# Kernel optimization log

Measured on AMD Instinct MI355X. Metric: run time of the kernel, lower is better.

## Reference

```python
import jax, jax.numpy as jnp
import numpy as np

C = 684      # encoder out_channels
H = 256      # hidden_size
I = 256      # input_size (embedding dim)
A = 512      # attention dim
V = 415      # word_num (vocab)
CCOV = 256   # coverage conv channels
K = 11       # coverage conv kernel
HF, WF = 32, 128  # feature map H', W'
RATIO = 16
T = 64       # fixed number of decode steps


def gru_cell(x, h, Wih, Whh, bih, bhh):
    # torch.nn.GRUCell semantics
    gi = x @ Wih.T + bih
    gh = h @ Whh.T + bhh
    ir, iz, inn = jnp.split(gi, 3, axis=-1)
    hr, hz, hn = jnp.split(gh, 3, axis=-1)
    r = jax.nn.sigmoid(ir + hr)
    z = jax.nn.sigmoid(iz + hz)
    n = jnp.tanh(inn + r * hn)
    return (1.0 - z) * n + z * h


def setup_inputs() -> dict:
    key = jax.random.key(0)
    ks = list(jax.random.split(key, 40))
    s = 0.05
    def rn(shape):
        return jax.random.normal(ks.pop(), shape, dtype=jnp.float32) * s
    p = {}
    p['cnn_features'] = jax.random.normal(ks.pop(), (1, C, HF, WF), dtype=jnp.float32)
    p['images_mask'] = jnp.ones((1, 1, HF * RATIO, WF * RATIO), dtype=jnp.float32)
    p['emb_table'] = rn((V, I))
    p['W_init'] = rn((H, C)); p['b_init'] = jnp.zeros((H,), jnp.float32)
    p['Wih_in'] = rn((3 * H, I)); p['Whh_in'] = rn((3 * H, H))
    p['bih_in'] = jnp.zeros((3 * H,), jnp.float32); p['bhh_in'] = jnp.zeros((3 * H,), jnp.float32)
    p['Wih_out'] = rn((3 * H, C)); p['Whh_out'] = rn((3 * H, H))
    p['bih_out'] = jnp.zeros((3 * H,), jnp.float32); p['bhh_out'] = jnp.zeros((3 * H,), jnp.float32)
    p['Wq'] = rn((A, H)); p['bq'] = jnp.zeros((A,), jnp.float32)
    p['Wproj'] = rn((A, C)); p['bproj'] = jnp.zeros((A,), jnp.float32)
    p['conv_k'] = rn((CCOV, 1, K, K))
    p['Wcov'] = rn((A, CCOV))
    p['wa'] = rn((A,)); p['ba'] = jnp.zeros((), jnp.float32)
    p['Ws'] = rn((H // 2, H)); p['bs'] = jnp.zeros((H // 2,), jnp.float32)
    p['We'] = rn((H // 2, I)); p['be'] = jnp.zeros((H // 2,), jnp.float32)
    p['Wc'] = rn((H // 2, C)); p['bc'] = jnp.zeros((H // 2,), jnp.float32)
    p['Wv'] = rn((V, H // 2)); p['bv'] = jnp.zeros((V,), jnp.float32)
    return p


def _decode(cnn_features, images_mask, emb_table, W_init, b_init,
            Wih_in, Whh_in, bih_in, bhh_in, Wih_out, Whh_out, bih_out, bhh_out,
            Wq, bq, Wproj, bproj, conv_k, Wcov, wa, ba,
            Ws, bs, We, be, Wc, bc, Wv, bv):
    mask = images_mask[:, :, ::RATIO, ::RATIO]          # [1,1,HF,WF]
    avg = jnp.sum(cnn_features * mask, axis=(2, 3)) / jnp.sum(mask, axis=(2, 3))  # [1,C]
    h0 = jnp.tanh(avg @ W_init.T + b_init)               # init_hidden
    cnn_trans = jnp.einsum('bchw,ac->bhwa', cnn_features, Wproj) + bproj  # 1x1 proj, [1,HF,WF,A]
    mask2d = mask[:, 0] > 0                              # [1,HF,WF]
    emb0 = emb_table[jnp.ones((1,), dtype=jnp.int32)]    # embedding(torch.ones(1).long())
    alpha_sum0 = jnp.zeros((1, 1, HF, WF), dtype=cnn_features.dtype)

    def attend(hidden, alpha_sum):
        q = hidden @ Wq.T + bq                           # [1,A]
        cov = jax.lax.conv_general_dilated(alpha_sum, conv_k, (1, 1), [(K // 2, K // 2)] * 2)
        cov_t = jnp.einsum('bchw,ac->bhwa', cov, Wcov)   # [1,HF,WF,A]
        e = jnp.tanh(q[:, None, None, :] + cov_t + cnn_trans)
        energy = jnp.einsum('bhwa,a->bhw', e, wa) + ba
        energy = jnp.where(mask2d, energy, -1e9)
        alpha = jax.nn.softmax(energy.reshape(1, -1), axis=-1).reshape(energy.shape)
        alpha_sum = alpha_sum + alpha[:, None]
        ctx = jnp.einsum('bhw,bchw->bc', alpha, cnn_features)  # [1,C]
        return ctx, alpha_sum

    def step(carry, _):
        emb, h_par, a_sum = carry
        h1 = gru_cell(emb, h_par, Wih_in, Whh_in, bih_in, bhh_in)      # word_input_gru
        ctx, a_sum = attend(h1, a_sum)                                  # word_attention
        h = gru_cell(ctx, h1, Wih_out, Whh_out, bih_out, bhh_out)       # word_out_gru
        state = (h @ Ws.T + bs) + (emb @ We.T + be) + (ctx @ Wc.T + bc) # fused out state
        prob = state @ Wv.T + bv                                        # word_convert, [1,V]
        word = jnp.argmax(prob, axis=-1)                                # greedy feedback
        emb_next = emb_table[word]
        return (emb_next, h, a_sum), prob[0]

    _, probs = jax.lax.scan(step, (emb0, h0, alpha_sum0), None, length=T)
    return probs  # [T, V]


def reference(cnn_features, images_mask, emb_table, W_init, b_init,
              Wih_in, Whh_in, bih_in, bhh_in, Wih_out, Whh_out, bih_out, bhh_out,
              Wq, bq, Wproj, bproj, conv_k, Wcov, wa, ba,
              Ws, bs, We, be, Wc, bc, Wv, bv):
    return _decode(cnn_features, images_mask, emb_table, W_init, b_init,
                   Wih_in, Whh_in, bih_in, bhh_in, Wih_out, Whh_out, bih_out, bhh_out,
                   Wq, bq, Wproj, bproj, conv_k, Wcov, wa, ba,
                   Ws, bs, We, be, Wc, bc, Wv, bv)
```

## Files before the change

### kernel.cpp

```cpp
#include <hip/hip_runtime.h>
#include <math.h>

#define HF 32
#define WF 128
#define HW 4096
#define C_DIM 684
#define H_DIM 256
#define A_DIM 512
#define V_DIM 415
#define PADR 42
#define PADC 144
#define T_STEPS 64

#define NERG 128
#define CTX0 128
#define NCTXB 86
#define MONO 214
#define TAIL0 215
#define GIO0 231
#define PSC0 247
#define NGRID 251

constexpr int CT_OFF      = 0;
constexpr int KMT_OFF     = CT_OFF + HW * A_DIM;
constexpr int APAD_OFF    = KMT_OFF + 61952;
constexpr int MASK_OFF    = APAD_OFF + 6048;
constexpr int PART_OFF    = MASK_OFF + 4096;
constexpr int AVG_OFF     = PART_OFF + 16384;
constexpr int H0_OFF      = AVG_OFF + 704;
constexpr int QV_OFF      = H0_OFF + 256;
constexpr int H1V_OFF     = QV_OFF + 512;
constexpr int GHOV_OFF    = H1V_OFF + 512;
constexpr int GHNV_OFF    = GHOV_OFF + 1536;
constexpr int GIOV_OFF    = GHNV_OFF + 768;
constexpr int PSCV_OFF    = GIOV_OFF + 768;
constexpr int CTXV_OFF    = PSCV_OFF + 128;
constexpr int MSUM_OFF    = CTXV_OFF + 704;
constexpr int FLAGS_OFF   = MSUM_OFF + 16;
constexpr int AFR_OFF     = FLAGS_OFF + 4096;
constexpr int CR_OFF      = AFR_OFF + 128;
constexpr int H1F_OFF     = CR_OFF + 128;
constexpr int TQR_OFF     = H1F_OFF + 128;
constexpr int SYNC_INTS   = 4096 + 128 + 128 + 128 + 2048;
constexpr int SYNC_END    = FLAGS_OFF + SYNC_INTS;
constexpr int GI_OFF      = SYNC_END;
constexpr int SE_OFF      = GI_OFF + V_DIM * 768;
constexpr int WST_OFF     = SE_OFF + V_DIM * 128;
constexpr int WVT_OFF     = WST_OFF + 256 * 128;
constexpr int WS_END      = WVT_OFF + 128 * V_DIM;

__device__ __forceinline__ float sigmoidf_(float x) { return 1.f / (1.f + expf(-x)); }
__device__ __forceinline__ float ftanh(float x) {
  float e = __expf(2.f * x);
  return 1.f - 2.f / (e + 1.f);
}

__device__ __forceinline__ float gld(const float* p) {
  int v = __hip_atomic_load((const int*)p, __ATOMIC_RELAXED, __HIP_MEMORY_SCOPE_AGENT);
  return __int_as_float(v);
}
__device__ __forceinline__ void gst(float* p, float x) {
  __hip_atomic_store((int*)p, __float_as_int(x), __ATOMIC_RELAXED, __HIP_MEMORY_SCOPE_AGENT);
}
__device__ __forceinline__ void pollf(int* p, int ph) {
  int it = 0;
  while (__hip_atomic_load(p, __ATOMIC_RELAXED, __HIP_MEMORY_SCOPE_AGENT) < ph) {
    if (it < 4) __builtin_amdgcn_s_sleep(1);
    else if (it < 16) __builtin_amdgcn_s_sleep(4);
    else __builtin_amdgcn_s_sleep(8);
    ++it;
  }
  asm volatile("" ::: "memory");
}
__device__ __forceinline__ void rel_store(int* p, int v) {
  __hip_atomic_store(p, v, __ATOMIC_RELEASE, __HIP_MEMORY_SCOPE_AGENT);
}


__global__ void k_init(const float* __restrict__ imask, float* ws) {
  __shared__ float red[4];
  int tid = threadIdx.x;
  float s = 0.f;
  for (int i = tid; i < HW; i += 256) {
    int h = i >> 7, w = i & 127;
    float m = imask[h * 16 * 2048 + w * 16];
    ws[MASK_OFF + i] = m;
    s += m;
  }
  for (int i = tid; i < PADR * PADC; i += 256) ws[APAD_OFF + i] = 0.f;
  int* sync = (int*)(ws + FLAGS_OFF);
  for (int i = tid; i < SYNC_INTS; i += 256) sync[i] = 0;
#pragma unroll
  for (int off = 32; off; off >>= 1) s += __shfl_xor(s, off, 64);
  if ((tid & 63) == 0) red[tid >> 6] = s;
  __syncthreads();
  if (tid == 0) ws[MSUM_OFF] = red[0] + red[1] + red[2] + red[3];
}

__global__ void k_avg(const float* __restrict__ cnn, float* ws) {
  __shared__ float red[4];
  int c = blockIdx.x, tid = threadIdx.x;
  const float* row = cnn + c * HW;
  float s = 0.f;
  for (int i = tid; i < HW; i += 256) s += ws[MASK_OFF + i] * row[i];
#pragma unroll
  for (int off = 32; off; off >>= 1) s += __shfl_xor(s, off, 64);
  if ((tid & 63) == 0) red[tid >> 6] = s;
  __syncthreads();
  if (tid == 0) ws[AVG_OFF + c] = (red[0] + red[1] + red[2] + red[3]) / ws[MSUM_OFF];
}

__global__ void k_h0(const float* __restrict__ W_init, const float* __restrict__ b_init, float* ws) {
  __shared__ float a_s[C_DIM];
  int tid = threadIdx.x;
  for (int i = tid; i < C_DIM; i += 256) a_s[i] = ws[AVG_OFF + i];
  __syncthreads();
  const float* wr = W_init + tid * C_DIM;
  float s = b_init[tid];
  for (int k = 0; k < C_DIM; k++) s += a_s[k] * wr[k];
  ws[H0_OFF + tid] = tanhf(s);
}

__global__ __launch_bounds__(512) void k_km(const float* __restrict__ convk,
                                            const float* __restrict__ Wcov, float* ws) {
  __shared__ float kt[256];
  int t = blockIdx.x, a = threadIdx.x;
  if (a < 256) kt[a] = convk[a * 121 + t];
  __syncthreads();
  const float* wr = Wcov + a * 256;
  float s = 0.f;
  for (int c = 0; c < 256; c++) s += kt[c] * wr[c];
  ws[KMT_OFF + a * 121 + t] = s;
}

__global__ void k_ct(const float* __restrict__ cnn, const float* __restrict__ Wproj,
                     const float* __restrict__ bproj, float* ws) {
  __shared__ float As[8][128];
  __shared__ float Bs[8][64];
  int hw0 = blockIdx.x * 128;
  int a0 = blockIdx.y * 64;
  int tid = threadIdx.x;
  int tx = tid & 15, ty = tid >> 4;
  float acc[8][4];
#pragma unroll
  for (int i = 0; i < 8; i++)
#pragma unroll
    for (int j = 0; j < 4; j++) acc[i][j] = 0.f;
  for (int c0 = 0; c0 < C_DIM; c0 += 8) {
    {
      int kk = tid >> 5;
      int m4 = (tid & 31) * 4;
      int c = c0 + kk;
      float4 v = make_float4(0.f, 0.f, 0.f, 0.f);
      if (c < C_DIM) v = *(const float4*)(cnn + c * HW + hw0 + m4);
      *(float4*)&As[kk][m4] = v;
    }
    {
      int n = tid & 63;
      int kk0 = (tid >> 6) * 2;
      const float* wr = Wproj + (a0 + n) * C_DIM + c0;
      Bs[kk0][n]     = (c0 + kk0 < C_DIM) ? wr[kk0] : 0.f;
      Bs[kk0 + 1][n] = (c0 + kk0 + 1 < C_DIM) ? wr[kk0 + 1] : 0.f;
    }
    __syncthreads();
#pragma unroll
    for (int kk = 0; kk < 8; kk++) {
      float a8[8], b4[4];
#pragma unroll
      for (int i = 0; i < 8; i++) a8[i] = As[kk][ty * 8 + i];
#pragma unroll
      for (int j = 0; j < 4; j++) b4[j] = Bs[kk][tx * 4 + j];
#pragma unroll
      for (int i = 0; i < 8; i++)
#pragma unroll
        for (int j = 0; j < 4; j++) acc[i][j] += a8[i] * b4[j];
    }
    __syncthreads();
  }
#pragma unroll
  for (int i = 0; i < 8; i++) {
    int hw = hw0 + ty * 8 + i;
#pragma unroll
    for (int j = 0; j < 4; j++) {
      int a = a0 + tx * 4 + j;
      ws[CT_OFF + hw * A_DIM + a] = acc[i][j] + bproj[a];
    }
  }
}

__global__ void k_gi(const float* __restrict__ emb_table, const float* __restrict__ Wih_in,
                     const float* __restrict__ bih_in, float* ws) {
  __shared__ float e_s[256];
  int v = blockIdx.x, tid = threadIdx.x;
  e_s[tid] = emb_table[v * 256 + tid];
  __syncthreads();
#pragma unroll
  for (int r = 0; r < 3; r++) {
    int m = r * 256 + tid;
    const float* wr = Wih_in + m * 256;
    float s = bih_in[m];
    for (int k = 0; k < 256; k++) s += e_s[k] * wr[k];
    ws[GI_OFF + v * 768 + m] = s;
  }
}

__global__ void k_se(const float* __restrict__ emb_table, const float* __restrict__ We,
                     const float* __restrict__ be, float* ws) {
  __shared__ float e_s[256];
  int v = blockIdx.x, tid = threadIdx.x;
  e_s[tid] = emb_table[v * 256 + tid];
  e_s[tid + 128] = emb_table[v * 256 + tid + 128];
  __syncthreads();
  const float* wr = We + tid * 256;
  float s = be[tid];
  for (int k = 0; k < 256; k++) s += e_s[k] * wr[k];
  ws[SE_OFF + v * 128 + tid] = s;
}

__global__ void k_tr(const float* __restrict__ in, float* __restrict__ out, int M, int Kd) {
  int total = M * Kd;
  for (int i = blockIdx.x * blockDim.x + threadIdx.x; i < total; i += gridDim.x * blockDim.x) {
    int m = i / Kd, k = i - m * Kd;
    out[k * M + m] = in[i];
  }
}

__global__ __launch_bounds__(512) void k_pre0(const float* __restrict__ Whh_in,
                                              const float* __restrict__ bhh_in, float* ws) {
  __shared__ float h0s[256];
  __shared__ float ghn48[48];
  const int s = blockIdx.x, tid = threadIdx.x;
  const int j0 = s * 16;
  if (tid < 256) h0s[tid] = ws[H0_OFF + tid];
  __syncthreads();
  {
    int r = tid >> 3, l = tid & 7;
    if (r < 48) {
      int mg = (r >> 4) * 256 + j0 + (r & 15);
      const float* wr = Whh_in + mg * 256 + l * 32;
      float sm = 0.f;
#pragma unroll
      for (int k = 0; k < 32; k++) sm += h0s[l * 32 + k] * wr[k];
#pragma unroll
      for (int off = 4; off; off >>= 1) sm += __shfl_xor(sm, off, 8);
      if (l == 0) ghn48[r] = sm + bhh_in[mg];
    }
  }
  __syncthreads();
  if (tid < 16) {
    int j = j0 + tid;
    const float* gi = ws + GI_OFF + 1 * 768;
    float r = sigmoidf_(gi[j] + ghn48[tid]);
    float z = sigmoidf_(gi[256 + j] + ghn48[16 + tid]);
    float n = tanhf(gi[512 + j] + r * ghn48[32 + tid]);
    gst(ws + H1V_OFF + j, (1.f - z) * n + z * h0s[j]);
  }
}

__global__ __launch_bounds__(512) void k_pre1(const float* __restrict__ Wq,
                                              const float* __restrict__ Whh_out,
                                              const float* __restrict__ bhh_out, float* ws) {
  __shared__ float h1s[256];
  const int s = blockIdx.x, tid = threadIdx.x;
  if (tid < 256) h1s[tid] = gld(ws + H1V_OFF + tid);
  __syncthreads();
  {
    int ap = tid >> 4, l = tid & 15;
    int a = s * 32 + ap;
    const float* wr = Wq + a * 256 + l * 16;
    float sm = 0.f;
#pragma unroll
    for (int k = 0; k < 16; k++) sm += h1s[l * 16 + k] * wr[k];
#pragma unroll
    for (int off = 8; off; off >>= 1) sm += __shfl_xor(sm, off, 16);
    if (l == 0) gst(ws + QV_OFF + a, sm);
  }
  {
    int r = tid >> 3, l = tid & 7;
    if (r < 48) {
      int m = s * 48 + r;
      const float* wr = Whh_out + m * 256 + l * 32;
      float sm = 0.f;
#pragma unroll
      for (int k = 0; k < 32; k++) sm += h1s[l * 32 + k] * wr[k];
#pragma unroll
      for (int off = 4; off; off >>= 1) sm += __shfl_xor(sm, off, 8);
      if (l == 0) gst(ws + GHOV_OFF + m, sm + bhh_out[m]);
    }
  }
}

__global__ void k_go(float* ws) {
  int tid = threadIdx.x;
  if (tid < 128) ((int*)(ws + TQR_OFF))[tid * 16] = 1;
}


__global__ __launch_bounds__(512) void k_steps(
    const float* __restrict__ cnn, const float* __restrict__ Whh_in,
    const float* __restrict__ Whh_out, const float* __restrict__ Wq,
    const float* __restrict__ Wih_out, const float* __restrict__ Wc_,
    const float* __restrict__ bq, const float* __restrict__ wa, const float* __restrict__ ba,
    const float* __restrict__ bih_out, const float* __restrict__ bhh_out,
    const float* __restrict__ bhh_in,
    const float* __restrict__ bs_, const float* __restrict__ bc_, const float* __restrict__ bv_,
    float* ws, float* __restrict__ out) {
  __shared__ __align__(16) float S[40016];

  const int bid = blockIdx.x, tid = threadIdx.x;
  int* flags = (int*)(ws + FLAGS_OFF);
  int* afr   = (int*)(ws + AFR_OFF);
  int* cr    = (int*)(ws + CR_OFF);
  int* h1f   = (int*)(ws + H1F_OFF);
  int* tqr   = (int*)(ws + TQR_OFF);

  if (bid < NERG) {
    const int h_row = bid >> 2, aq = bid & 3, a0 = aq * 128;
    const int al = tid & 127, hslot = tid >> 7;
    float* km    = S;
    float* ct    = S + 16896;
    float* patch = S + 33280;
    float* maskv = S + 34864;
    float* redE  = S + 34992;
    for (int i = tid; i < 128 * 132; i += 512) {
      int a = i / 132, j = i - a * 132;
      int dy = j / 12, dx = j - dy * 12;
      km[i] = (dx < 11) ? ws[KMT_OFF + (a0 + a) * 121 + dy * 11 + dx] : 0.f;
    }
    for (int i = tid; i < 128 * 128; i += 512) {
      int w = i >> 7, aa = i & 127;
      ct[i] = ws[CT_OFF + (h_row * 128 + w) * 512 + a0 + aa];
    }
    if (tid < 128) maskv[tid] = ws[MASK_OFF + h_row * 128 + tid];
    const float bq_a = bq[a0 + al], wa_a = wa[a0 + al], ba0 = ba[0];
    __syncthreads();

#pragma unroll 1
    for (int t = 0; t < T_STEPS; t++) {
      if (tid == 0) pollf(&cr[(bid & 7) * 16], t);
      __syncthreads();
      for (int i = tid; i < 11 * 138; i += 512) {
        int r = i / 138, c = i - r * 138;
        patch[r * 144 + c] = gld(ws + APAD_OFF + (h_row + r) * PADC + c);
      }
      __syncthreads();
      float acc[2][16];
#pragma unroll
      for (int p = 0; p < 2; p++)
#pragma unroll
        for (int i = 0; i < 16; i++) acc[p][i] = 0.f;
      const int wbase0 = hslot * 32;
#pragma unroll 1
      for (int dy = 0; dy < 11; dy++) {
        float kv[12];
        {
          const float* kb = &km[al * 132 + dy * 12];
          *(float4*)&kv[0] = *(const float4*)&kb[0];
          *(float4*)&kv[4] = *(const float4*)&kb[4];
          *(float4*)&kv[8] = *(const float4*)&kb[8];
        }
#pragma unroll
        for (int p = 0; p < 2; p++) {
          float row[28];
          const float* pr = &patch[dy * 144 + wbase0 + p * 16];
#pragma unroll
          for (int i = 0; i < 7; i++) *(float4*)&row[i * 4] = *(const float4*)&pr[i * 4];
#pragma unroll
          for (int dx = 0; dx < 11; dx++)
#pragma unroll
            for (int wi = 0; wi < 16; wi++) acc[p][wi] += kv[dx] * row[wi + dx];
        }
      }
      if (tid < 16) pollf(&tqr[(tid * 8 + (bid & 7)) * 16], t + 1);
      __syncthreads();
      float qa = bq_a + gld(ws + QV_OFF + a0 + al);
#pragma unroll 1
      for (int p = 0; p < 2; p++) {
        const int wbase = wbase0 + p * 16;
#pragma unroll
        for (int wi = 0; wi < 16; wi++) {
          float x = acc[p][wi] + qa + ct[(wbase + wi) * 128 + al];
          float v = ftanh(x) * wa_a;
#pragma unroll
          for (int off = 32; off; off >>= 1) v += __shfl_xor(v, off, 64);
          if ((tid & 63) == 0) redE[(tid >> 6) * 16 + wi] = v;
        }
        __syncthreads();
        if (tid < 64) {
          int hs2 = tid >> 4, wi = tid & 15;
          int w = hs2 * 32 + p * 16 + wi;
          float e = redE[(hs2 * 2) * 16 + wi] + redE[(hs2 * 2 + 1) * 16 + wi];
          float val = (maskv[w] > 0.f) ? (e + (aq == 0 ? ba0 : 0.f)) : -2.5e8f;
          gst(ws + PART_OFF + aq * 4096 + h_row * 128 + w, val);
        }
        __syncthreads();
      }
      if (tid == 0) rel_store(&flags[bid * 16], t + 1);
    }

  } else if (bid < CTX0 + NCTXB) {
    const int cb = bid - CTX0, c0 = cb * 8;
    float* cnnS = S;
    float* redC = S + 32768;
    float* ctxv = S + 32832;
    float* invp = S + 32840;
    for (int i = tid; i < 8 * 4096; i += 512) {
      int c = c0 + (i >> 12);
      cnnS[i] = (c < C_DIM) ? cnn[c * 4096 + (i & 4095)] : 0.f;
    }
    __syncthreads();

#pragma unroll 1
    for (int t = 0; t < T_STEPS; t++) {
      if (tid == 0) pollf(&afr[(bid & 7) * 16], t + 1);
      __syncthreads();
      float ev[8];
      float ssum = 0.f;
#pragma unroll
      for (int j = 0; j < 8; j++) {
        int hw = j * 512 + tid;
        float e = gld(ws + PART_OFF + hw) + gld(ws + PART_OFF + 4096 + hw) +
                  gld(ws + PART_OFF + 8192 + hw) + gld(ws + PART_OFF + 12288 + hw);
        ev[j] = __expf(e);
        ssum += ev[j];
      }
#pragma unroll
      for (int off = 32; off; off >>= 1) ssum += __shfl_xor(ssum, off, 64);
      if ((tid & 63) == 0) redC[tid >> 6] = ssum;
      __syncthreads();
      if (tid == 0) {
        float s2 = 0.f;
#pragma unroll
        for (int i = 0; i < 8; i++) s2 += redC[i];
        invp[0] = 1.f / s2;
      }
      __syncthreads();
      float inv = invp[0];
      if (cb < 8) {
        int hw = cb * 512 + tid;
        int hh = hw >> 7, ww = hw & 127;
        float* ap = ws + APAD_OFF + (hh + 5) * PADC + ww + 5;
        gst(ap, gld(ap) + ev[cb] * inv);
      }
#pragma unroll
      for (int cc = 0; cc < 8; cc++) {
        float p = 0.f;
#pragma unroll
        for (int j = 0; j < 8; j++) p += ev[j] * cnnS[cc * 4096 + j * 512 + tid];
#pragma unroll
        for (int off = 32; off; off >>= 1) p += __shfl_xor(p, off, 64);
        if ((tid & 63) == 0) redC[(tid >> 6) * 8 + cc] = p;
      }
      __syncthreads();
      if (tid < 8) {
        float cv = 0.f;
#pragma unroll
        for (int w2 = 0; w2 < 8; w2++) cv += redC[w2 * 8 + tid];
        gst(ws + CTXV_OFF + c0 + tid, cv * inv);
      }
      __syncthreads();
      if (tid == 0) rel_store(&flags[(CTX0 + cb) * 16], t + 1);
    }

  } else if (bid == MONO) {
    float* wst  = S;
    float* mh   = S + 32768;
    float* mst  = S + 33024;
    float* wval = S + 33152;
    int*   widx = (int*)(S + 33160);
    int*   mwp  = (int*)(S + 33168);
    int*   mwn  = (int*)(S + 33169);
    for (int i = tid; i < 256 * 128; i += 512) wst[i] = ws[WST_OFF + i];
    if (tid == 0) mwp[0] = 1;
    __syncthreads();

#pragma unroll 1
    for (int t = 0; t < T_STEPS; t++) {
      const int par = t & 1;
      if (tid < 128) pollf(&flags[tid * 16], t + 1);
      __syncthreads();
      if (tid < 8) rel_store(&afr[tid * 16], t + 1);
      float o0 = 0.f, o1 = 0.f, o2 = 0.f, h1v = 0.f;
      if (tid < 256) {
        const float* gh = ws + GHOV_OFF + par * 768;
        o0 = gld(gh + tid);
        o1 = gld(gh + 256 + tid);
        o2 = gld(gh + 512 + tid);
        h1v = gld(ws + H1V_OFF + par * 256 + tid);
      }
      if (tid < NCTXB) pollf(&flags[(CTX0 + tid) * 16], t + 1);
      __syncthreads();
      if (tid < 8) rel_store(&cr[tid * 16], t + 1);
      if (tid < 16) pollf(&flags[(230 + tid) * 16], t + 1);
      else if (tid < 20) pollf(&flags[(246 + tid - 16) * 16], t + 1);
      __syncthreads();
      if (tid < 256) {
        float g0 = gld(ws + GIOV_OFF + tid);
        float g1 = gld(ws + GIOV_OFF + 256 + tid);
        float g2 = gld(ws + GIOV_OFF + 512 + tid);
        float r = sigmoidf_(g0 + o0);
        float z = sigmoidf_(g1 + o1);
        float n = tanhf(g2 + r * o2);
        mh[tid] = (1.f - z) * n + z * h1v;
      }
      __syncthreads();
      if (tid < 128) {
        float s = bs_[tid] + bc_[tid] + ws[SE_OFF + mwp[0] * 128 + tid] +
                  gld(ws + PSCV_OFF + tid);
        const float* wt = wst + tid;
#pragma unroll 8
        for (int k = 0; k < 256; k++) s += mh[k] * wt[k * 128];
        mst[tid] = s;
      }
      __syncthreads();
      {
        float best = -3.4e38f;
        int bi = tid;
        if (tid < V_DIM) {
          float p2 = bv_[tid];
          const float* wt = ws + WVT_OFF + tid;
#pragma unroll 8
          for (int k = 0; k < 128; k++) p2 += mst[k] * wt[k * V_DIM];
          out[t * V_DIM + tid] = p2;
          best = p2;
        }
#pragma unroll
        for (int off = 32; off; off >>= 1) {
          float ov = __shfl_xor(best, off, 64);
          int oi = __shfl_xor(bi, off, 64);
          if (ov > best || (ov == best && oi < bi)) { best = ov; bi = oi; }
        }
        if ((tid & 63) == 0) { wval[tid >> 6] = best; widx[tid >> 6] = bi; }
        __syncthreads();
        if (tid == 0) {
          float b0 = wval[0];
          int i0 = widx[0];
          for (int w2 = 1; w2 < 8; w2++) {
            if (wval[w2] > b0 || (wval[w2] == b0 && widx[w2] < i0)) {
              b0 = wval[w2];
              i0 = widx[w2];
            }
          }
          mwn[0] = i0;
        }
        __syncthreads();
      }
      if (tid < 16) pollf(&flags[(214 + tid) * 16], t + 1);
      __syncthreads();
      if (tid < 256) {
        const float* gi = ws + GI_OFF + mwn[0] * 768;
        float n0 = gld(ws + GHNV_OFF + tid);
        float n1 = gld(ws + GHNV_OFF + 256 + tid);
        float n2 = gld(ws + GHNV_OFF + 512 + tid);
        float r = sigmoidf_(gi[tid] + n0);
        float z = sigmoidf_(gi[256 + tid] + n1);
        float n = tanhf(gi[512 + tid] + r * n2);
        gst(ws + H1V_OFF + ((t + 1) & 1) * 256 + tid, (1.f - z) * n + z * mh[tid]);
      }
      __syncthreads();
      if (tid < 8) rel_store(&h1f[tid * 16], t + 1);
      if (tid == 0) mwp[0] = mwn[0];
      __syncthreads();
    }

  } else if (bid < GIO0) {
    const int s = bid - TAIL0;
    float* whinS = S;
    float* whoS  = S + 12672;
    float* wqS   = S + 25344;
    float* hS    = S + 33792;
    float* h1S   = S + 34048;
    for (int i = tid; i < 48 * 256; i += 512) whinS[(i >> 8) * 264 + (i & 255)] = Whh_in[s * 12288 + i];
    for (int i = tid; i < 48 * 256; i += 512) whoS[(i >> 8) * 264 + (i & 255)] = Whh_out[s * 12288 + i];
    for (int i = tid; i < 32 * 256; i += 512) wqS[(i >> 8) * 264 + (i & 255)] = Wq[s * 8192 + i];
    __syncthreads();

#pragma unroll 1
    for (int t = 0; t < T_STEPS; t++) {
      const int par = t & 1;
      if (tid < 16) pollf(&flags[(230 + tid) * 16], t + 1);
      __syncthreads();
      if (tid < 256) {
        float g0 = gld(ws + GIOV_OFF + tid);
        float g1 = gld(ws + GIOV_OFF + 256 + tid);
        float g2 = gld(ws + GIOV_OFF + 512 + tid);
        const float* gh = ws + GHOV_OFF + par * 768;
        float o0 = gld(gh + tid), o1 = gld(gh + 256 + tid), o2 = gld(gh + 512 + tid);
        float h1v = gld(ws + H1V_OFF + par * 256 + tid);
        float r = sigmoidf_(g0 + o0);
        float z = sigmoidf_(g1 + o1);
        float n = tanhf(g2 + r * o2);
        hS[tid] = (1.f - z) * n + z * h1v;
      }
      __syncthreads();
      {
        int r = tid >> 3, l = tid & 7;
        if (r < 48) {
          int m = s * 48 + r;
          float sm = 0.f;
#pragma unroll
          for (int jj = 0; jj < 8; jj++) {
            float4 w4 = *(const float4*)&whinS[r * 264 + jj * 32 + l * 4];
            float4 h4 = *(const float4*)&hS[jj * 32 + l * 4];
            sm += w4.x * h4.x + w4.y * h4.y + w4.z * h4.z + w4.w * h4.w;
          }
#pragma unroll
          for (int off = 4; off; off >>= 1) sm += __shfl_xor(sm, off, 8);
          if (l == 0) gst(ws + GHNV_OFF + m, sm + bhh_in[m]);
        }
      }
      __syncthreads();
      if (tid == 0) rel_store(&flags[(214 + s) * 16], t + 1);
      if (tid == 0) pollf(&h1f[(s & 7) * 16], t + 1);
      __syncthreads();
      if (tid < 256) h1S[tid] = gld(ws + H1V_OFF + ((t + 1) & 1) * 256 + tid);
      __syncthreads();
      {
        int r = tid >> 3, l = tid & 7;
        if (r < 48) {
          int m = s * 48 + r;
          float sm = 0.f;
#pragma unroll
          for (int jj = 0; jj < 8; jj++) {
            float4 w4 = *(const float4*)&whoS[r * 264 + jj * 32 + l * 4];
            float4 h4 = *(const float4*)&h1S[jj * 32 + l * 4];
            sm += w4.x * h4.x + w4.y * h4.y + w4.z * h4.z + w4.w * h4.w;
          }
#pragma unroll
          for (int off = 4; off; off >>= 1) sm += __shfl_xor(sm, off, 8);
          if (l == 0) gst(ws + GHOV_OFF + ((t + 1) & 1) * 768 + m, sm + bhh_out[m]);
        }
      }
      {
        int ap = tid >> 4, l = tid & 15;
        int a = s * 32 + ap;
        float sm = 0.f;
#pragma unroll
        for (int jj = 0; jj < 4; jj++) {
          float4 w4 = *(const float4*)&wqS[ap * 264 + jj * 64 + l * 4];
          float4 h4 = *(const float4*)&h1S[jj * 64 + l * 4];
          sm += w4.x * h4.x + w4.y * h4.y + w4.z * h4.z + w4.w * h4.w;
        }
#pragma unroll
        for (int off = 8; off; off >>= 1) sm += __shfl_xor(sm, off, 16);
        if (l == 0) gst(ws + QV_OFF + a, sm);
      }
      __syncthreads();
      if (tid < 8) rel_store(&tqr[(s * 8 + tid) * 16], t + 2);
    }

  } else if (bid < PSC0) {
    const int g = bid - GIO0;
    float* wS  = S;
    float* cvS = S + 33120;
    for (int i = tid; i < 48 * 684; i += 512) {
      int r = i / 684, c = i - r * 684;
      wS[r * 690 + c] = Wih_out[(g * 48 + r) * 684 + c];
    }
    __syncthreads();
#pragma unroll 1
    for (int t = 0; t < T_STEPS; t++) {
      if (tid == 0) pollf(&cr[(bid & 7) * 16], t + 1);
      __syncthreads();
      for (int i = tid; i < 684; i += 512) cvS[i] = gld(ws + CTXV_OFF + i);
      __syncthreads();
      {
        int r = tid >> 3, l = tid & 7;
        if (r < 48) {
          float sm = 0.f;
          for (int k = l; k < 684; k += 8) sm += wS[r * 690 + k] * cvS[k];
#pragma unroll
          for (int off = 4; off; off >>= 1) sm += __shfl_xor(sm, off, 8);
          if (l == 0) {
            int m = g * 48 + r;
            gst(ws + GIOV_OFF + m, sm + bih_out[m]);
          }
        }
      }
      __syncthreads();
      if (tid == 0) rel_store(&flags[(230 + g) * 16], t + 1);
    }

  } else {
    const int p = bid - PSC0;
    float* wS  = S;
    float* cvS = S + 22080;
    for (int i = tid; i < 32 * 684; i += 512) {
      int r = i / 684, c = i - r * 684;
      wS[r * 690 + c] = Wc_[(p * 32 + r) * 684 + c];
    }
    __syncthreads();
#pragma unroll 1
    for (int t = 0; t < T_STEPS; t++) {
      if (tid == 0) pollf(&cr[(bid & 7) * 16], t + 1);
      __syncthreads();
      for (int i = tid; i < 684; i += 512) cvS[i] = gld(ws + CTXV_OFF + i);
      __syncthreads();
      {
        int r = tid >> 4, l = tid & 15;
        if (r < 32) {
          float sm = 0.f;
          for (int k = l; k < 684; k += 16) sm += wS[r * 690 + k] * cvS[k];
#pragma unroll
          for (int off = 8; off; off >>= 1) sm += __shfl_xor(sm, off, 16);
          if (l == 0) gst(ws + PSCV_OFF + p * 32 + r, sm);
        }
      }
      __syncthreads();
      if (tid == 0) rel_store(&flags[(246 + p) * 16], t + 1);
    }
  }
}


extern "C" void kernel_launch(void* const* d_in, const int* in_sizes, int n_in,
                              void* d_out, int out_size, void* d_ws, size_t ws_size,
                              hipStream_t stream) {
  (void)in_sizes; (void)n_in; (void)out_size; (void)ws_size;
  const float* cnn      = (const float*)d_in[0];
  const float* imask    = (const float*)d_in[1];
  const float* emb_tab  = (const float*)d_in[2];
  const float* W_init   = (const float*)d_in[3];
  const float* b_init   = (const float*)d_in[4];
  const float* Wih_in   = (const float*)d_in[5];
  const float* Whh_in   = (const float*)d_in[6];
  const float* bih_in   = (const float*)d_in[7];
  const float* bhh_in   = (const float*)d_in[8];
  const float* Wih_out  = (const float*)d_in[9];
  const float* Whh_out  = (const float*)d_in[10];
  const float* bih_out  = (const float*)d_in[11];
  const float* bhh_out  = (const float*)d_in[12];
  const float* Wq       = (const float*)d_in[13];
  const float* bq       = (const float*)d_in[14];
  const float* Wproj    = (const float*)d_in[15];
  const float* bproj    = (const float*)d_in[16];
  const float* convk    = (const float*)d_in[17];
  const float* Wcov     = (const float*)d_in[18];
  const float* Ws_      = (const float*)d_in[21];
  const float* bs_      = (const float*)d_in[22];
  const float* We_      = (const float*)d_in[23];
  const float* be_      = (const float*)d_in[24];
  const float* Wc_      = (const float*)d_in[25];
  const float* bc_      = (const float*)d_in[26];
  const float* Wv_      = (const float*)d_in[27];
  const float* bv_      = (const float*)d_in[28];
  const float* wa       = (const float*)d_in[19];
  const float* ba       = (const float*)d_in[20];
  float* ws  = (float*)d_ws;
  float* out = (float*)d_out;

  k_init<<<1, 256, 0, stream>>>(imask, ws);
  k_avg<<<C_DIM, 256, 0, stream>>>(cnn, ws);
  k_h0<<<1, 256, 0, stream>>>(W_init, b_init, ws);
  k_km<<<121, 512, 0, stream>>>(convk, Wcov, ws);
  k_ct<<<dim3(HW / 128, A_DIM / 64), 256, 0, stream>>>(cnn, Wproj, bproj, ws);
  k_gi<<<V_DIM, 256, 0, stream>>>(emb_tab, Wih_in, bih_in, ws);
  k_se<<<V_DIM, 128, 0, stream>>>(emb_tab, We_, be_, ws);
  k_tr<<<512, 256, 0, stream>>>(Ws_, ws + WST_OFF, 128, 256);
  k_tr<<<512, 256, 0, stream>>>(Wv_, ws + WVT_OFF, 415, 128);
  k_pre0<<<16, 512, 0, stream>>>(Whh_in, bhh_in, ws);
  k_pre1<<<16, 512, 0, stream>>>(Wq, Whh_out, bhh_out, ws);
  k_go<<<1, 256, 0, stream>>>(ws);

  k_steps<<<NGRID, 512, 0, stream>>>(cnn, Whh_in, Whh_out, Wq, Wih_out, Wc_,
                                     bq, wa, ba, bih_out, bhh_out, bhh_in,
                                     bs_, bc_, bv_, ws, out);
}
```

Before: 2.750 ms.

## Replace relay-based step barriers with direct replicated producer flags

Removes the MONO block's relay stage, where it polled all energy and context flags and then republished them as aggregate flags. Energy blocks now write 8 replicated flags, which context blocks poll directly. Context blocks write 8 replicated flags, which the GRU-gate, psc and MONO blocks poll directly. This cuts a serial hop from each step's critical path, at the cost of more flag stores and wider polling per block.

```diff
diff --git a/kernel.cpp b/kernel.cpp
--- a/kernel.cpp
+++ b/kernel.cpp
@@ -36,13 +36,16 @@
 constexpr int PSCV_OFF    = GIOV_OFF + 768;
 constexpr int CTXV_OFF    = PSCV_OFF + 128;
 constexpr int MSUM_OFF    = CTXV_OFF + 704;
-constexpr int FLAGS_OFF   = MSUM_OFF + 16;
-constexpr int AFR_OFF     = FLAGS_OFF + 4096;
-constexpr int CR_OFF      = AFR_OFF + 128;
-constexpr int H1F_OFF     = CR_OFF + 128;
-constexpr int TQR_OFF     = H1F_OFF + 128;
-constexpr int SYNC_INTS   = 4096 + 128 + 128 + 128 + 2048;
-constexpr int SYNC_END    = FLAGS_OFF + SYNC_INTS;
+constexpr int EFR_OFF     = MSUM_OFF + 16;
+constexpr int CFR_OFF     = EFR_OFF + 1024 * 16;
+constexpr int TF_OFF      = CFR_OFF + 688 * 16;
+constexpr int GF_OFF      = TF_OFF + 16 * 16;
+constexpr int PSCF_OFF    = GF_OFF + 16 * 16;
+constexpr int CR_OFF      = PSCF_OFF + 4 * 16;
+constexpr int H1F_OFF     = CR_OFF + 8 * 16;
+constexpr int TQR_OFF     = H1F_OFF + 8 * 16;
+constexpr int SYNC_INTS   = (1024 + 688 + 16 + 16 + 4 + 8 + 8 + 128) * 16;
+constexpr int SYNC_END    = EFR_OFF + SYNC_INTS;
 constexpr int GI_OFF      = SYNC_END;
 constexpr int SE_OFF      = GI_OFF + V_DIM * 768;
 constexpr int WST_OFF     = SE_OFF + V_DIM * 128;
@@ -88,7 +91,7 @@
     s += m;
   }
   for (int i = tid; i < PADR * PADC; i += 256) ws[APAD_OFF + i] = 0.f;
-  int* sync = (int*)(ws + FLAGS_OFF);
+  int* sync = (int*)(ws + EFR_OFF);
   for (int i = tid; i < SYNC_INTS; i += 256) sync[i] = 0;
 #pragma unroll
   for (int off = 32; off; off >>= 1) s += __shfl_xor(s, off, 64);
@@ -308,11 +311,14 @@
   __shared__ __align__(16) float S[40016];
 
   const int bid = blockIdx.x, tid = threadIdx.x;
-  int* flags = (int*)(ws + FLAGS_OFF);
-  int* afr   = (int*)(ws + AFR_OFF);
-  int* cr    = (int*)(ws + CR_OFF);
-  int* h1f   = (int*)(ws + H1F_OFF);
-  int* tqr   = (int*)(ws + TQR_OFF);
+  int* efr  = (int*)(ws + EFR_OFF);
+  int* cfr  = (int*)(ws + CFR_OFF);
+  int* tf   = (int*)(ws + TF_OFF);
+  int* gf   = (int*)(ws + GF_OFF);
+  int* pscf = (int*)(ws + PSCF_OFF);
+  int* cr   = (int*)(ws + CR_OFF);
+  int* h1f  = (int*)(ws + H1F_OFF);
+  int* tqr  = (int*)(ws + TQR_OFF);
 
   if (bid < NERG) {
     const int h_row = bid >> 2, aq = bid & 3, a0 = aq * 128;
@@ -395,7 +401,7 @@
         }
         __syncthreads();
       }
-      if (tid == 0) rel_store(&flags[bid * 16], t + 1);
+      if (tid < 8) rel_store(&efr[(bid * 8 + tid) * 16], t + 1);
     }
 
   } else if (bid < CTX0 + NCTXB) {
@@ -412,7 +418,7 @@
 
 #pragma unroll 1
     for (int t = 0; t < T_STEPS; t++) {
-      if (tid == 0) pollf(&afr[(bid & 7) * 16], t + 1);
+      if (tid < 128) pollf(&efr[(tid * 8 + (cb & 7)) * 16], t + 1);
       __syncthreads();
       float ev[8];
       float ssum = 0.f;
@@ -459,7 +465,7 @@
         gst(ws + CTXV_OFF + c0 + tid, cv * inv);
       }
       __syncthreads();
-      if (tid == 0) rel_store(&flags[(CTX0 + cb) * 16], t + 1);
+      if (tid < 8) rel_store(&cfr[(cb * 8 + tid) * 16], t + 1);
     }
 
   } else if (bid == MONO) {
@@ -477,9 +483,9 @@
 #pragma unroll 1
     for (int t = 0; t < T_STEPS; t++) {
       const int par = t & 1;
-      if (tid < 128) pollf(&flags[tid * 16], t + 1);
-      __syncthreads();
-      if (tid < 8) rel_store(&afr[tid * 16], t + 1);
+      if (tid < NCTXB) pollf(&cfr[(tid * 8 + 7) * 16], t + 1);
+      __syncthreads();
+      if (tid < 8) rel_store(&cr[tid * 16], t + 1);
       float o0 = 0.f, o1 = 0.f, o2 = 0.f, h1v = 0.f;
       if (tid < 256) {
         const float* gh = ws + GHOV_OFF + par * 768;
@@ -488,11 +494,8 @@
         o2 = gld(gh + 512 + tid);
         h1v = gld(ws + H1V_OFF + par * 256 + tid);
       }
-      if (tid < NCTXB) pollf(&flags[(CTX0 + tid) * 16], t + 1);
-      __syncthreads();
-      if (tid < 8) rel_store(&cr[tid * 16], t + 1);
-      if (tid < 16) pollf(&flags[(230 + tid) * 16], t + 1);
-      else if (tid < 20) pollf(&flags[(246 + tid - 16) * 16], t + 1);
+      if (tid < 16) pollf(&gf[tid * 16], t + 1);
+      else if (tid < 20) pollf(&pscf[(tid - 16) * 16], t + 1);
       __syncthreads();
       if (tid < 256) {
         float g0 = gld(ws + GIOV_OFF + tid);
@@ -545,7 +548,7 @@
         }
         __syncthreads();
       }
-      if (tid < 16) pollf(&flags[(214 + tid) * 16], t + 1);
+      if (tid < 16) pollf(&tf[tid * 16], t + 1);
       __syncthreads();
       if (tid < 256) {
         const float* gi = ws + GI_OFF + mwn[0] * 768;
@@ -578,7 +581,7 @@
 #pragma unroll 1
     for (int t = 0; t < T_STEPS; t++) {
       const int par = t & 1;
-      if (tid < 16) pollf(&flags[(230 + tid) * 16], t + 1);
+      if (tid < 16) pollf(&gf[tid * 16], t + 1);
       __syncthreads();
       if (tid < 256) {
         float g0 = gld(ws + GIOV_OFF + tid);
@@ -610,7 +613,7 @@
         }
       }
       __syncthreads();
-      if (tid == 0) rel_store(&flags[(214 + s) * 16], t + 1);
+      if (tid == 0) rel_store(&tf[s * 16], t + 1);
       if (tid == 0) pollf(&h1f[(s & 7) * 16], t + 1);
       __syncthreads();
       if (tid < 256) h1S[tid] = gld(ws + H1V_OFF + ((t + 1) & 1) * 256 + tid);
@@ -660,7 +663,7 @@
     __syncthreads();
 #pragma unroll 1
     for (int t = 0; t < T_STEPS; t++) {
-      if (tid == 0) pollf(&cr[(bid & 7) * 16], t + 1);
+      if (tid < NCTXB) pollf(&cfr[(tid * 8 + (bid & 7)) * 16], t + 1);
       __syncthreads();
       for (int i = tid; i < 684; i += 512) cvS[i] = gld(ws + CTXV_OFF + i);
       __syncthreads();
@@ -678,7 +681,7 @@
         }
       }
       __syncthreads();
-      if (tid == 0) rel_store(&flags[(230 + g) * 16], t + 1);
+      if (tid == 0) rel_store(&gf[g * 16], t + 1);
     }
 
   } else {
@@ -692,7 +695,7 @@
     __syncthreads();
 #pragma unroll 1
     for (int t = 0; t < T_STEPS; t++) {
-      if (tid == 0) pollf(&cr[(bid & 7) * 16], t + 1);
+      if (tid < NCTXB) pollf(&cfr[(tid * 8 + (bid & 7)) * 16], t + 1);
       __syncthreads();
       for (int i = tid; i < 684; i += 512) cvS[i] = gld(ws + CTXV_OFF + i);
       __syncthreads();
@@ -707,7 +710,7 @@
         }
       }
       __syncthreads();
-      if (tid == 0) rel_store(&flags[(246 + p) * 16], t + 1);
+      if (tid == 0) rel_store(&pscf[p * 16], t + 1);
     }
   }
 }
@@ -736,6 +739,8 @@
   const float* bproj    = (const float*)d_in[16];
   const float* convk    = (const float*)d_in[17];
   const float* Wcov     = (const float*)d_in[18];
+  const float* wa       = (const float*)d_in[19];
+  const float* ba       = (const float*)d_in[20];
   const float* Ws_      = (const float*)d_in[21];
   const float* bs_      = (const float*)d_in[22];
   const float* We_      = (const float*)d_in[23];
@@ -744,8 +749,6 @@
   const float* bc_      = (const float*)d_in[26];
   const float* Wv_      = (const float*)d_in[27];
   const float* bv_      = (const float*)d_in[28];
-  const float* wa       = (const float*)d_in[19];
-  const float* ba       = (const float*)d_in[20];
   float* ws  = (float*)d_ws;
   float* out = (float*)d_out;
 
```

After: 2.734 ms. Within noise of the previous version (-0.6%).
